# Kernel tuning notes

Hardware: AMD Instinct MI355X
Metric: run time of the kernel (lower is better)

The kernel has to match this reference:

```python
import jax, jax.numpy as jnp
import numpy as np

N, D, V, T = 1024, 64, 32000, 2048
U_DECAY = 0.97
LN_EPS = 1e-6


def _layernorm_row(z):
    # matches torch: (z - mean) / (std_unbiased + eps), std uses ddof=1
    m = z.mean(axis=-1, keepdims=True)
    s = jnp.std(z, axis=-1, ddof=1, keepdims=True)
    return (z - m) / (s + LN_EPS)


def setup_inputs() -> dict:
    key = jax.random.key(0)
    k1, k2, k3, k4, k5 = jax.random.split(key, 5)
    E = jax.random.normal(k1, (D, N), dtype=jnp.float32) / np.float32(np.sqrt(N))
    Dx = jax.random.normal(k2, (N, D), dtype=jnp.float32) / np.float32(np.sqrt(D))
    Dy = jax.random.normal(k3, (N, D), dtype=jnp.float32) / np.float32(np.sqrt(D))
    token_emb = jax.random.normal(k4, (V, D), dtype=jnp.float32) / np.float32(np.sqrt(D))
    tokens = jax.random.randint(k5, (T,), 0, V, dtype=jnp.int32)
    x0 = jnp.zeros((N,), dtype=jnp.float32)
    rho0 = jnp.zeros((D, N), dtype=jnp.float32)
    return {"E": E, "Dx": Dx, "Dy": Dy, "token_emb": token_emb,
            "x0": x0, "rho0": rho0, "tokens": tokens}


def reference(E, Dx, Dy, token_emb, x0, rho0, tokens):
    def step(carry, tok):
        x, rho = carry                        # x: [N], rho: [D, N]
        v_prev = token_emb[tok]               # [D]
        x_t = x + jax.nn.relu(Dx @ v_prev)    # [N], use_relu_lowrank=True
        a_star = rho @ x_t                    # [D]
        y_core = Dy @ _layernorm_row(a_star)  # ln_before_Dy=True -> [N]
        y_t = jax.nn.relu(y_core) * jax.nn.relu(x_t)  # [N]
        v_star = _layernorm_row(E @ y_t)      # [D]
        rho_new = U_DECAY * (rho + jnp.outer(v_prev, x_t))  # [D, N]
        return (x_t, rho_new), (y_t, v_star)

    (_, _), (ys, vs) = jax.lax.scan(step, (x0, rho0), tokens)
    return ys, vs  # [T, N], [T, D]
```

## Files before the change

kernel.cpp:

```cpp
#include <hip/hip_runtime.h>
#include <math.h>

#define NN 1024
#define DD 64
#define TT 2048
#define UDEC 0.97f
#define EPS 1e-6f
#define CC 64
#define NCH 32
#define NSL 8
#define SLW 128
#define C2 32
#define NC2 64

__global__ __launch_bounds__(256) void k_xscan(
    const float* __restrict__ Dx, const float* __restrict__ temb,
    const int* __restrict__ toks, float* __restrict__ Xp, float* __restrict__ S)
{
    const int cs = blockIdx.y;
    const int n  = blockIdx.x * 256 + threadIdx.x;
    __shared__ float Vs[C2][DD];
    for (int i = threadIdx.x; i < C2 * DD; i += 256) {
        int s = i >> 6, d = i & 63;
        Vs[s][d] = temb[toks[cs * C2 + s] * DD + d];
    }
    __syncthreads();
    float dxr[DD];
    const float4* dx4 = reinterpret_cast<const float4*>(Dx + n * DD);
#pragma unroll
    for (int j = 0; j < DD / 4; ++j) {
        float4 v = dx4[j];
        dxr[4*j] = v.x; dxr[4*j+1] = v.y; dxr[4*j+2] = v.z; dxr[4*j+3] = v.w;
    }
    float run = 0.f;
    for (int s = 0; s < C2; ++s) {
        const float4* vr = reinterpret_cast<const float4*>(&Vs[s][0]);
        float a0 = 0.f, a1 = 0.f, a2 = 0.f, a3 = 0.f;
#pragma unroll
        for (int j = 0; j < DD / 4; ++j) {
            float4 v = vr[j];
            a0 += v.x * dxr[4*j];     a1 += v.y * dxr[4*j+1];
            a2 += v.z * dxr[4*j+2];   a3 += v.w * dxr[4*j+3];
        }
        float r = (a0 + a1) + (a2 + a3);
        run += fmaxf(r, 0.f);
        Xp[(cs * C2 + s) * NN + n] = run;
    }
    S[cs * NN + n] = run;
}

__global__ __launch_bounds__(256) void k_base(
    const float* __restrict__ S, const float* __restrict__ x0, float* __restrict__ Bb)
{
    const int n = blockIdx.x * 256 + threadIdx.x;
    float acc = x0[n];
    for (int cs = 0; cs < NC2; ++cs) {
        Bb[cs * NN + n] = acc;
        acc += S[cs * NN + n];
    }
}


__global__ __launch_bounds__(256) void k_M(
    const float* __restrict__ Xp, const float* __restrict__ Bb,
    const float* __restrict__ temb, const int* __restrict__ toks, float* __restrict__ M)
{
    const int c = blockIdx.y, q = blockIdx.x;
    __shared__ float Xs[CC][SLW + 1];
    __shared__ float Vw[CC][DD];
    __shared__ float pw[CC + 1];
    const int tid = threadIdx.x;
    if (tid <= CC) pw[tid] = powf(UDEC, (float)tid);
    __syncthreads();
    for (int i = tid; i < CC * SLW; i += 256) {
        int s = i / SLW, n = i % SLW;
        int t = c * CC + s, gn = q * SLW + n;
        Xs[s][n] = Xp[t * NN + gn] + Bb[(t >> 5) * NN + gn];
    }
    for (int i = tid; i < CC * DD; i += 256) {
        int s = i >> 6, d = i & 63;
        Vw[s][d] = temb[toks[c * CC + s] * DD + d] * pw[CC - s];
    }
    __syncthreads();
    const int n_l = tid & 127;
    const int dh  = tid >> 7;
    float acc[32];
#pragma unroll
    for (int k = 0; k < 32; ++k) acc[k] = 0.f;
    for (int s = 0; s < CC; ++s) {
        float xv = Xs[s][n_l];
        const float4* vr = reinterpret_cast<const float4*>(&Vw[s][dh * 32]);
#pragma unroll
        for (int k8 = 0; k8 < 8; ++k8) {
            float4 v = vr[k8];
            acc[4*k8]   += v.x * xv;  acc[4*k8+1] += v.y * xv;
            acc[4*k8+2] += v.z * xv;  acc[4*k8+3] += v.w * xv;
        }
    }
    for (int k = 0; k < 32; ++k)
        M[(c * DD + dh * 32 + k) * NN + q * SLW + n_l] = acc[k];
}

__global__ __launch_bounds__(256) void k_rho(
    const float* __restrict__ M, const float* __restrict__ rho0, float* __restrict__ Rho)
{
    const int el = blockIdx.x * 256 + threadIdx.x;
    float acc = rho0[el];
    const float uc = powf(UDEC, (float)CC);
    for (int c = 0; c < NCH; ++c) {
        Rho[c * (DD * NN) + el] = acc;
        acc = fmaf(acc, uc, M[c * (DD * NN) + el]);
    }
}

__global__ __launch_bounds__(256) void k_gram(
    const float* __restrict__ Xp, const float* __restrict__ Bb,
    const float* __restrict__ Rho, float* __restrict__ Gp, float* __restrict__ Pp)
{
    const int c = blockIdx.y, q = blockIdx.x;
    __shared__ float Xs[CC][SLW + 1];
    __shared__ float Rs[DD][SLW + 1];
    const int tid = threadIdx.x;
    for (int i = tid; i < CC * SLW; i += 256) {
        int s = i / SLW, n = i % SLW;
        int t = c * CC + s, gn = q * SLW + n;
        Xs[s][n] = Xp[t * NN + gn] + Bb[(t >> 5) * NN + gn];
        Rs[s][n] = Rho[(c * DD + s) * NN + gn];
    }
    __syncthreads();
    const int ti = tid >> 4;
    const int sj = tid & 15;
    float acc[16];
#pragma unroll
    for (int k = 0; k < 16; ++k) acc[k] = 0.f;
    for (int n = 0; n < SLW; ++n) {
        float xt[4], xs[4];
#pragma unroll
        for (int a = 0; a < 4; ++a) xt[a] = Xs[ti * 4 + a][n];
#pragma unroll
        for (int b = 0; b < 4; ++b) xs[b] = Xs[sj * 4 + b][n];
#pragma unroll
        for (int a = 0; a < 4; ++a)
#pragma unroll
            for (int b = 0; b < 4; ++b) acc[a * 4 + b] += xt[a] * xs[b];
    }
    {
        float* base = Gp + ((size_t)(c * NSL + q) * CC) * CC;
#pragma unroll
        for (int a = 0; a < 4; ++a)
            *reinterpret_cast<float4*>(base + (ti * 4 + a) * CC + sj * 4) =
                make_float4(acc[a*4], acc[a*4+1], acc[a*4+2], acc[a*4+3]);
    }
#pragma unroll
    for (int k = 0; k < 16; ++k) acc[k] = 0.f;
    for (int n = 0; n < SLW; ++n) {
        float xt[4], rv[4];
#pragma unroll
        for (int a = 0; a < 4; ++a) xt[a] = Xs[ti * 4 + a][n];
#pragma unroll
        for (int b = 0; b < 4; ++b) rv[b] = Rs[sj * 4 + b][n];
#pragma unroll
        for (int a = 0; a < 4; ++a)
#pragma unroll
            for (int b = 0; b < 4; ++b) acc[a * 4 + b] += xt[a] * rv[b];
    }
    {
        float* base = Pp + ((size_t)(c * NSL + q) * CC) * DD;
#pragma unroll
        for (int a = 0; a < 4; ++a)
            *reinterpret_cast<float4*>(base + (ti * 4 + a) * DD + sj * 4) =
                make_float4(acc[a*4], acc[a*4+1], acc[a*4+2], acc[a*4+3]);
    }
}

__global__ __launch_bounds__(256) void k_astar(
    const float* __restrict__ Gp, const float* __restrict__ Pp,
    const float* __restrict__ temb, const int* __restrict__ toks,
    float* __restrict__ LNA)
{
    const int c = blockIdx.x;
    __shared__ float G[CC][CC + 1];
    __shared__ float P[CC][DD + 1];
    __shared__ float Ve[CC][DD];
    __shared__ float As[CC][DD + 1];
    __shared__ float pw[CC + 1];
    __shared__ float mrow[CC], srow[CC];
    const int tid = threadIdx.x;
    if (tid <= CC) pw[tid] = powf(UDEC, (float)tid);
    for (int i = tid; i < CC * CC; i += 256) {
        int t = i >> 6, s = i & 63;
        float ag = 0.f, ap = 0.f;
#pragma unroll
        for (int qq = 0; qq < NSL; ++qq) {
            ag += Gp[((size_t)(c * NSL + qq) * CC + t) * CC + s];
            ap += Pp[((size_t)(c * NSL + qq) * CC + t) * DD + s];
        }
        G[t][s] = ag; P[t][s] = ap;
    }
    for (int i = tid; i < CC * DD; i += 256) {
        int s = i >> 6, d = i & 63;
        Ve[s][d] = temb[toks[c * CC + s] * DD + d];
    }
    __syncthreads();
    const int t_l = tid >> 2;
    const int qq  = tid & 3;
    float acc[16];
#pragma unroll
    for (int j = 0; j < 16; ++j) acc[j] = pw[t_l] * P[t_l][qq * 16 + j];
    for (int s = 0; s < t_l; ++s) {
        float wv = pw[t_l - s] * G[t_l][s];
        const float4* ver = reinterpret_cast<const float4*>(&Ve[s][qq * 16]);
#pragma unroll
        for (int k = 0; k < 4; ++k) {
            float4 v = ver[k];
            acc[4*k]   += wv * v.x;  acc[4*k+1] += wv * v.y;
            acc[4*k+2] += wv * v.z;  acc[4*k+3] += wv * v.w;
        }
    }
#pragma unroll
    for (int j = 0; j < 16; ++j) As[t_l][qq * 16 + j] = acc[j];
    __syncthreads();
    if (tid < CC) {
        float m = 0.f;
#pragma unroll
        for (int d = 0; d < DD; ++d) m += As[tid][d];
        m *= (1.f / DD);
        float v = 0.f;
#pragma unroll
        for (int d = 0; d < DD; ++d) { float z = As[tid][d] - m; v += z * z; }
        mrow[tid] = m;
        srow[tid] = 1.f / (sqrtf(v / (DD - 1)) + EPS);
    }
    __syncthreads();
    for (int i = tid; i < CC * DD; i += 256) {
        int t = i >> 6, d = i & 63;
        LNA[(c * CC + t) * DD + d] = (As[t][d] - mrow[t]) * srow[t];
    }
}

__global__ __launch_bounds__(256) void k_y(
    const float* __restrict__ LNA, const float* __restrict__ Dy,
    const float* __restrict__ Xp, const float* __restrict__ Bb,
    float* __restrict__ ys)
{
    const int tt = blockIdx.y;
    const int n  = blockIdx.x * 256 + threadIdx.x;
    __shared__ float L[8][DD];
    for (int i = threadIdx.x; i < 8 * DD; i += 256) L[i >> 6][i & 63] = LNA[tt * 8 * DD + i];
    __syncthreads();
    float dyr[DD];
    const float4* dy4 = reinterpret_cast<const float4*>(Dy + n * DD);
#pragma unroll
    for (int j = 0; j < 16; ++j) {
        float4 v = dy4[j];
        dyr[4*j] = v.x; dyr[4*j+1] = v.y; dyr[4*j+2] = v.z; dyr[4*j+3] = v.w;
    }
#pragma unroll
    for (int t = 0; t < 8; ++t) {
        const float4* lr = reinterpret_cast<const float4*>(&L[t][0]);
        float a0 = 0.f, a1 = 0.f, a2 = 0.f, a3 = 0.f;
#pragma unroll
        for (int j = 0; j < 16; ++j) {
            float4 v = lr[j];
            a0 += v.x * dyr[4*j];   a1 += v.y * dyr[4*j+1];
            a2 += v.z * dyr[4*j+2]; a3 += v.w * dyr[4*j+3];
        }
        float yc = (a0 + a1) + (a2 + a3);
        int tg = tt * 8 + t;
        float xv = Xp[tg * NN + n] + Bb[(tg >> 5) * NN + n];
        ys[tg * NN + n] = fmaxf(yc, 0.f) * fmaxf(xv, 0.f);
    }
}

__global__ __launch_bounds__(256) void k_v(
    const float* __restrict__ ys, const float* __restrict__ E, float* __restrict__ vs)
{
    const int tt = blockIdx.x;
    __shared__ float Ys[8][NN];
    __shared__ float pre[8][DD + 1];
    __shared__ float mrow[8], srow[8];
    const int tid = threadIdx.x;
    for (int i = tid; i < 8 * NN; i += 256) Ys[i >> 10][i & 1023] = ys[tt * 8 * NN + i];
    __syncthreads();
    const int d  = tid & 63;
    const int tq = tid >> 6;
    const int t0 = tq * 2;
    const float4* e4 = reinterpret_cast<const float4*>(E + d * NN);
    float a00=0,a01=0,a02=0,a03=0, a10=0,a11=0,a12=0,a13=0;
    for (int j = 0; j < NN / 4; ++j) {
        float4 ev  = e4[j];
        float4 y0v = *reinterpret_cast<const float4*>(&Ys[t0][4 * j]);
        float4 y1v = *reinterpret_cast<const float4*>(&Ys[t0 + 1][4 * j]);
        a00 += ev.x * y0v.x; a01 += ev.y * y0v.y; a02 += ev.z * y0v.z; a03 += ev.w * y0v.w;
        a10 += ev.x * y1v.x; a11 += ev.y * y1v.y; a12 += ev.z * y1v.z; a13 += ev.w * y1v.w;
    }
    pre[t0][d]     = (a00 + a01) + (a02 + a03);
    pre[t0 + 1][d] = (a10 + a11) + (a12 + a13);
    __syncthreads();
    if (tid < 8) {
        float m = 0.f;
#pragma unroll
        for (int dd2 = 0; dd2 < DD; ++dd2) m += pre[tid][dd2];
        m *= (1.f / DD);
        float v = 0.f;
#pragma unroll
        for (int dd2 = 0; dd2 < DD; ++dd2) { float z = pre[tid][dd2] - m; v += z * z; }
        mrow[tid] = m;
        srow[tid] = 1.f / (sqrtf(v / (DD - 1)) + EPS);
    }
    __syncthreads();
    for (int i = tid; i < 8 * DD; i += 256) {
        int t = i >> 6, dd2 = i & 63;
        vs[(tt * 8 + t) * DD + dd2] = (pre[t][dd2] - mrow[t]) * srow[t];
    }
}

extern "C" void kernel_launch(void* const* d_in, const int* in_sizes, int n_in,
                              void* d_out, int out_size, void* d_ws, size_t ws_size,
                              hipStream_t stream) {
    (void)in_sizes; (void)n_in; (void)out_size; (void)ws_size;
    const float* E    = (const float*)d_in[0];
    const float* Dx   = (const float*)d_in[1];
    const float* Dy   = (const float*)d_in[2];
    const float* temb = (const float*)d_in[3];
    const float* x0   = (const float*)d_in[4];
    const float* rho0 = (const float*)d_in[5];
    const int*   toks = (const int*)d_in[6];

    float* ys = (float*)d_out;
    float* vs = ys + (size_t)TT * NN;

    float* w   = (float*)d_ws;
    float* Xp  = w;
    float* S   = Xp  + (size_t)TT * NN;
    float* Bb  = S   + (size_t)NC2 * NN;
    float* M   = Bb  + (size_t)NC2 * NN;
    float* Rho = M   + (size_t)NCH * DD * NN;
    float* LNA = Rho + (size_t)NCH * DD * NN;
    float* Gp = M;
    float* Pp = M + (size_t)NCH * NSL * CC * CC;

    k_xscan<<<dim3(4, NC2),  256, 0, stream>>>(Dx, temb, toks, Xp, S);
    k_base <<<dim3(4),       256, 0, stream>>>(S, x0, Bb);
    k_M    <<<dim3(NSL, NCH),256, 0, stream>>>(Xp, Bb, temb, toks, M);
    k_rho  <<<dim3(DD*NN/256),256,0, stream>>>(M, rho0, Rho);
    k_gram <<<dim3(NSL, NCH),256, 0, stream>>>(Xp, Bb, Rho, Gp, Pp);
    k_astar<<<dim3(NCH),     256, 0, stream>>>(Gp, Pp, temb, toks, LNA);
    k_y    <<<dim3(4, TT/8), 256, 0, stream>>>(LNA, Dy, Xp, Bb, ys);
    k_v    <<<dim3(TT/8),    256, 0, stream>>>(ys, E, vs);
}
```

Before: 194.7 us.

## Fuse all stages into one persistent kernel with grid-wide barriers

```diff
diff --git a/kernel.cpp b/kernel.cpp
--- a/kernel.cpp
+++ b/kernel.cpp
@@ -13,305 +13,297 @@
 #define C2 32
 #define NC2 64
 
-__global__ __launch_bounds__(256) void k_xscan(
-    const float* __restrict__ Dx, const float* __restrict__ temb,
-    const int* __restrict__ toks, float* __restrict__ Xp, float* __restrict__ S)
+#define NBLK 256
+#define NTHR 256
+
+struct SmP1 { float Vs[C2][DD]; };
+struct SmP3 { float Xs[CC][SLW + 1]; float Vw[CC][DD]; float pw[CC + 1]; };
+struct SmP5 { float Xs[CC][65]; float Rs[CC][65]; };
+struct SmP6 { float Ve[CC][DD]; float Gt[8][CC]; float Pt[8][DD]; float pw[CC + 1]; };
+struct SmP7 { float Ys[8][NN]; float L[8][DD]; float pre[8][DD + 1]; float mrow[8]; float srow[8]; };
+#define SMEM_BYTES 50176
+
+__device__ __forceinline__ void gridbar(unsigned* cnt, unsigned target) {
+    __syncthreads();
+    if (threadIdx.x == 0) {
+        __builtin_amdgcn_fence(__ATOMIC_RELEASE, "agent");
+        atomicAdd(cnt, 1u);
+        int spins = 0;
+        while (__hip_atomic_load(cnt, __ATOMIC_RELAXED, __HIP_MEMORY_SCOPE_AGENT) < target) {
+            __builtin_amdgcn_s_sleep(2);
+            if (++spins > (1 << 22)) break;
+        }
+        __builtin_amdgcn_fence(__ATOMIC_ACQUIRE, "agent");
+    }
+    __syncthreads();
+}
+
+__global__ __launch_bounds__(NTHR) void fused_bdh(
+    const float* __restrict__ E, const float* __restrict__ Dx,
+    const float* __restrict__ Dy, const float* __restrict__ temb,
+    const float* __restrict__ x0, const float* __restrict__ rho0,
+    const int* __restrict__ toks,
+    float* __restrict__ ys, float* __restrict__ vs,
+    float* __restrict__ Xp, float* __restrict__ S, float* __restrict__ Bb,
+    float* __restrict__ M, float* __restrict__ Rho, float* __restrict__ LNA,
+    float* __restrict__ Gp, float* __restrict__ Pp, unsigned* __restrict__ bar)
 {
-    const int cs = blockIdx.y;
-    const int n  = blockIdx.x * 256 + threadIdx.x;
-    __shared__ float Vs[C2][DD];
-    for (int i = threadIdx.x; i < C2 * DD; i += 256) {
-        int s = i >> 6, d = i & 63;
-        Vs[s][d] = temb[toks[cs * C2 + s] * DD + d];
-    }
-    __syncthreads();
-    float dxr[DD];
-    const float4* dx4 = reinterpret_cast<const float4*>(Dx + n * DD);
-#pragma unroll
-    for (int j = 0; j < DD / 4; ++j) {
-        float4 v = dx4[j];
-        dxr[4*j] = v.x; dxr[4*j+1] = v.y; dxr[4*j+2] = v.z; dxr[4*j+3] = v.w;
-    }
-    float run = 0.f;
-    for (int s = 0; s < C2; ++s) {
-        const float4* vr = reinterpret_cast<const float4*>(&Vs[s][0]);
-        float a0 = 0.f, a1 = 0.f, a2 = 0.f, a3 = 0.f;
-#pragma unroll
-        for (int j = 0; j < DD / 4; ++j) {
-            float4 v = vr[j];
-            a0 += v.x * dxr[4*j];     a1 += v.y * dxr[4*j+1];
-            a2 += v.z * dxr[4*j+2];   a3 += v.w * dxr[4*j+3];
-        }
-        float r = (a0 + a1) + (a2 + a3);
-        run += fmaxf(r, 0.f);
-        Xp[(cs * C2 + s) * NN + n] = run;
-    }
-    S[cs * NN + n] = run;
-}
-
-__global__ __launch_bounds__(256) void k_base(
-    const float* __restrict__ S, const float* __restrict__ x0, float* __restrict__ Bb)
-{
-    const int n = blockIdx.x * 256 + threadIdx.x;
-    float acc = x0[n];
-    for (int cs = 0; cs < NC2; ++cs) {
-        Bb[cs * NN + n] = acc;
-        acc += S[cs * NN + n];
-    }
-}
-
-
-__global__ __launch_bounds__(256) void k_M(
-    const float* __restrict__ Xp, const float* __restrict__ Bb,
-    const float* __restrict__ temb, const int* __restrict__ toks, float* __restrict__ M)
-{
-    const int c = blockIdx.y, q = blockIdx.x;
-    __shared__ float Xs[CC][SLW + 1];
-    __shared__ float Vw[CC][DD];
-    __shared__ float pw[CC + 1];
-    const int tid = threadIdx.x;
-    if (tid <= CC) pw[tid] = powf(UDEC, (float)tid);
-    __syncthreads();
-    for (int i = tid; i < CC * SLW; i += 256) {
-        int s = i / SLW, n = i % SLW;
-        int t = c * CC + s, gn = q * SLW + n;
-        Xs[s][n] = Xp[t * NN + gn] + Bb[(t >> 5) * NN + gn];
-    }
-    for (int i = tid; i < CC * DD; i += 256) {
-        int s = i >> 6, d = i & 63;
-        Vw[s][d] = temb[toks[c * CC + s] * DD + d] * pw[CC - s];
-    }
-    __syncthreads();
-    const int n_l = tid & 127;
-    const int dh  = tid >> 7;
-    float acc[32];
-#pragma unroll
-    for (int k = 0; k < 32; ++k) acc[k] = 0.f;
-    for (int s = 0; s < CC; ++s) {
-        float xv = Xs[s][n_l];
-        const float4* vr = reinterpret_cast<const float4*>(&Vw[s][dh * 32]);
-#pragma unroll
-        for (int k8 = 0; k8 < 8; ++k8) {
-            float4 v = vr[k8];
-            acc[4*k8]   += v.x * xv;  acc[4*k8+1] += v.y * xv;
-            acc[4*k8+2] += v.z * xv;  acc[4*k8+3] += v.w * xv;
-        }
-    }
-    for (int k = 0; k < 32; ++k)
-        M[(c * DD + dh * 32 + k) * NN + q * SLW + n_l] = acc[k];
-}
-
-__global__ __launch_bounds__(256) void k_rho(
-    const float* __restrict__ M, const float* __restrict__ rho0, float* __restrict__ Rho)
-{
-    const int el = blockIdx.x * 256 + threadIdx.x;
-    float acc = rho0[el];
-    const float uc = powf(UDEC, (float)CC);
-    for (int c = 0; c < NCH; ++c) {
-        Rho[c * (DD * NN) + el] = acc;
-        acc = fmaf(acc, uc, M[c * (DD * NN) + el]);
-    }
-}
-
-__global__ __launch_bounds__(256) void k_gram(
-    const float* __restrict__ Xp, const float* __restrict__ Bb,
-    const float* __restrict__ Rho, float* __restrict__ Gp, float* __restrict__ Pp)
-{
-    const int c = blockIdx.y, q = blockIdx.x;
-    __shared__ float Xs[CC][SLW + 1];
-    __shared__ float Rs[DD][SLW + 1];
-    const int tid = threadIdx.x;
-    for (int i = tid; i < CC * SLW; i += 256) {
-        int s = i / SLW, n = i % SLW;
-        int t = c * CC + s, gn = q * SLW + n;
-        Xs[s][n] = Xp[t * NN + gn] + Bb[(t >> 5) * NN + gn];
-        Rs[s][n] = Rho[(c * DD + s) * NN + gn];
-    }
-    __syncthreads();
-    const int ti = tid >> 4;
-    const int sj = tid & 15;
-    float acc[16];
-#pragma unroll
-    for (int k = 0; k < 16; ++k) acc[k] = 0.f;
-    for (int n = 0; n < SLW; ++n) {
-        float xt[4], xs[4];
-#pragma unroll
-        for (int a = 0; a < 4; ++a) xt[a] = Xs[ti * 4 + a][n];
-#pragma unroll
-        for (int b = 0; b < 4; ++b) xs[b] = Xs[sj * 4 + b][n];
-#pragma unroll
-        for (int a = 0; a < 4; ++a)
-#pragma unroll
-            for (int b = 0; b < 4; ++b) acc[a * 4 + b] += xt[a] * xs[b];
-    }
-    {
-        float* base = Gp + ((size_t)(c * NSL + q) * CC) * CC;
-#pragma unroll
-        for (int a = 0; a < 4; ++a)
-            *reinterpret_cast<float4*>(base + (ti * 4 + a) * CC + sj * 4) =
-                make_float4(acc[a*4], acc[a*4+1], acc[a*4+2], acc[a*4+3]);
-    }
-#pragma unroll
-    for (int k = 0; k < 16; ++k) acc[k] = 0.f;
-    for (int n = 0; n < SLW; ++n) {
-        float xt[4], rv[4];
-#pragma unroll
-        for (int a = 0; a < 4; ++a) xt[a] = Xs[ti * 4 + a][n];
-#pragma unroll
-        for (int b = 0; b < 4; ++b) rv[b] = Rs[sj * 4 + b][n];
-#pragma unroll
-        for (int a = 0; a < 4; ++a)
-#pragma unroll
-            for (int b = 0; b < 4; ++b) acc[a * 4 + b] += xt[a] * rv[b];
-    }
-    {
+    extern __shared__ __align__(16) char smem[];
+    const int b = blockIdx.x, tid = threadIdx.x;
+
+    {
+        SmP1* sm = (SmP1*)smem;
+        const int cs = b >> 2, qx = b & 3;
+        const int n = qx * 256 + tid;
+        for (int i = tid; i < C2 * DD; i += NTHR) {
+            int s = i >> 6, d = i & 63;
+            sm->Vs[s][d] = temb[toks[cs * C2 + s] * DD + d];
+        }
+        __syncthreads();
+        float dxr[DD];
+        const float4* dx4 = reinterpret_cast<const float4*>(Dx + n * DD);
+#pragma unroll
+        for (int j = 0; j < 16; ++j) {
+            float4 v = dx4[j];
+            dxr[4*j] = v.x; dxr[4*j+1] = v.y; dxr[4*j+2] = v.z; dxr[4*j+3] = v.w;
+        }
+        float run = 0.f;
+        for (int s = 0; s < C2; ++s) {
+            const float4* vr = reinterpret_cast<const float4*>(&sm->Vs[s][0]);
+            float a0 = 0.f, a1 = 0.f, a2 = 0.f, a3 = 0.f;
+#pragma unroll
+            for (int j = 0; j < 16; ++j) {
+                float4 v = vr[j];
+                a0 += v.x * dxr[4*j];     a1 += v.y * dxr[4*j+1];
+                a2 += v.z * dxr[4*j+2];   a3 += v.w * dxr[4*j+3];
+            }
+            run += fmaxf((a0 + a1) + (a2 + a3), 0.f);
+            Xp[(cs * C2 + s) * NN + n] = run;
+        }
+        S[cs * NN + n] = run;
+    }
+    gridbar(bar, 1 * NBLK);
+
+    if (b < 4) {
+        const int n = b * 256 + tid;
+        float acc = x0[n];
+        for (int cs = 0; cs < NC2; ++cs) {
+            Bb[cs * NN + n] = acc;
+            acc += S[cs * NN + n];
+        }
+    }
+    gridbar(bar, 2 * NBLK);
+
+    {
+        SmP3* sm = (SmP3*)smem;
+        const int c = b >> 3, q = b & 7;
+        if (tid <= CC) sm->pw[tid] = powf(UDEC, (float)tid);
+        __syncthreads();
+        for (int i = tid; i < CC * SLW; i += NTHR) {
+            int s = i >> 7, n = i & 127;
+            int t = c * CC + s, gn = q * SLW + n;
+            sm->Xs[s][n] = Xp[t * NN + gn] + Bb[(t >> 5) * NN + gn];
+        }
+        for (int i = tid; i < CC * DD; i += NTHR) {
+            int s = i >> 6, d = i & 63;
+            sm->Vw[s][d] = temb[toks[c * CC + s] * DD + d] * sm->pw[CC - s];
+        }
+        __syncthreads();
+        {
+            const int n_l = tid & 127, dh = tid >> 7;
+            float acc[32];
+#pragma unroll
+            for (int k = 0; k < 32; ++k) acc[k] = 0.f;
+            for (int s = 0; s < CC; ++s) {
+                float xv = sm->Xs[s][n_l];
+                const float4* vr = reinterpret_cast<const float4*>(&sm->Vw[s][dh * 32]);
+#pragma unroll
+                for (int k8 = 0; k8 < 8; ++k8) {
+                    float4 v = vr[k8];
+                    acc[4*k8]   += v.x * xv;  acc[4*k8+1] += v.y * xv;
+                    acc[4*k8+2] += v.z * xv;  acc[4*k8+3] += v.w * xv;
+                }
+            }
+            for (int k = 0; k < 32; ++k)
+                M[(c * DD + dh * 32 + k) * NN + q * SLW + n_l] = acc[k];
+        }
+        {
+            const int ti = tid >> 4, sj = tid & 15;
+            float acc[16];
+#pragma unroll
+            for (int k = 0; k < 16; ++k) acc[k] = 0.f;
+            for (int n = 0; n < SLW; ++n) {
+                float xt[4], xs[4];
+#pragma unroll
+                for (int a = 0; a < 4; ++a) xt[a] = sm->Xs[ti * 4 + a][n];
+#pragma unroll
+                for (int e2 = 0; e2 < 4; ++e2) xs[e2] = sm->Xs[sj * 4 + e2][n];
+#pragma unroll
+                for (int a = 0; a < 4; ++a)
+#pragma unroll
+                    for (int e2 = 0; e2 < 4; ++e2) acc[a * 4 + e2] += xt[a] * xs[e2];
+            }
+            float* base = Gp + ((size_t)(c * NSL + q) * CC) * CC;
+#pragma unroll
+            for (int a = 0; a < 4; ++a)
+                *reinterpret_cast<float4*>(base + (ti * 4 + a) * CC + sj * 4) =
+                    make_float4(acc[a*4], acc[a*4+1], acc[a*4+2], acc[a*4+3]);
+        }
+    }
+    gridbar(bar, 3 * NBLK);
+
+    {
+        const int el = b * NTHR + tid;
+        float acc = rho0[el];
+        const float uc = powf(UDEC, (float)CC);
+        for (int c = 0; c < NCH; ++c) {
+            Rho[c * (DD * NN) + el] = acc;
+            acc = fmaf(acc, uc, M[c * (DD * NN) + el]);
+        }
+    }
+    gridbar(bar, 4 * NBLK);
+
+    {
+        SmP5* sm = (SmP5*)smem;
+        const int c = b >> 3, q = b & 7;
+        const int ti = tid >> 4, sj = tid & 15;
+        float acc[16];
+#pragma unroll
+        for (int k = 0; k < 16; ++k) acc[k] = 0.f;
+        for (int h = 0; h < 2; ++h) {
+            __syncthreads();
+            for (int i = tid; i < CC * 64; i += NTHR) {
+                int s = i >> 6, n = i & 63;
+                int t = c * CC + s, gn = q * SLW + h * 64 + n;
+                sm->Xs[s][n] = Xp[t * NN + gn] + Bb[(t >> 5) * NN + gn];
+                sm->Rs[s][n] = Rho[(c * DD + s) * NN + gn];
+            }
+            __syncthreads();
+            for (int n = 0; n < 64; ++n) {
+                float xt[4], rv[4];
+#pragma unroll
+                for (int a = 0; a < 4; ++a) xt[a] = sm->Xs[ti * 4 + a][n];
+#pragma unroll
+                for (int e2 = 0; e2 < 4; ++e2) rv[e2] = sm->Rs[sj * 4 + e2][n];
+#pragma unroll
+                for (int a = 0; a < 4; ++a)
+#pragma unroll
+                    for (int e2 = 0; e2 < 4; ++e2) acc[a * 4 + e2] += xt[a] * rv[e2];
+            }
+        }
         float* base = Pp + ((size_t)(c * NSL + q) * CC) * DD;
 #pragma unroll
         for (int a = 0; a < 4; ++a)
             *reinterpret_cast<float4*>(base + (ti * 4 + a) * DD + sj * 4) =
                 make_float4(acc[a*4], acc[a*4+1], acc[a*4+2], acc[a*4+3]);
     }
-}
-
-__global__ __launch_bounds__(256) void k_astar(
-    const float* __restrict__ Gp, const float* __restrict__ Pp,
-    const float* __restrict__ temb, const int* __restrict__ toks,
-    float* __restrict__ LNA)
-{
-    const int c = blockIdx.x;
-    __shared__ float G[CC][CC + 1];
-    __shared__ float P[CC][DD + 1];
-    __shared__ float Ve[CC][DD];
-    __shared__ float As[CC][DD + 1];
-    __shared__ float pw[CC + 1];
-    __shared__ float mrow[CC], srow[CC];
-    const int tid = threadIdx.x;
-    if (tid <= CC) pw[tid] = powf(UDEC, (float)tid);
-    for (int i = tid; i < CC * CC; i += 256) {
-        int t = i >> 6, s = i & 63;
-        float ag = 0.f, ap = 0.f;
-#pragma unroll
-        for (int qq = 0; qq < NSL; ++qq) {
-            ag += Gp[((size_t)(c * NSL + qq) * CC + t) * CC + s];
-            ap += Pp[((size_t)(c * NSL + qq) * CC + t) * DD + s];
-        }
-        G[t][s] = ag; P[t][s] = ap;
-    }
-    for (int i = tid; i < CC * DD; i += 256) {
-        int s = i >> 6, d = i & 63;
-        Ve[s][d] = temb[toks[c * CC + s] * DD + d];
-    }
-    __syncthreads();
-    const int t_l = tid >> 2;
-    const int qq  = tid & 3;
-    float acc[16];
-#pragma unroll
-    for (int j = 0; j < 16; ++j) acc[j] = pw[t_l] * P[t_l][qq * 16 + j];
-    for (int s = 0; s < t_l; ++s) {
-        float wv = pw[t_l - s] * G[t_l][s];
-        const float4* ver = reinterpret_cast<const float4*>(&Ve[s][qq * 16]);
-#pragma unroll
-        for (int k = 0; k < 4; ++k) {
-            float4 v = ver[k];
-            acc[4*k]   += wv * v.x;  acc[4*k+1] += wv * v.y;
-            acc[4*k+2] += wv * v.z;  acc[4*k+3] += wv * v.w;
-        }
-    }
-#pragma unroll
-    for (int j = 0; j < 16; ++j) As[t_l][qq * 16 + j] = acc[j];
-    __syncthreads();
-    if (tid < CC) {
-        float m = 0.f;
-#pragma unroll
-        for (int d = 0; d < DD; ++d) m += As[tid][d];
-        m *= (1.f / DD);
-        float v = 0.f;
-#pragma unroll
-        for (int d = 0; d < DD; ++d) { float z = As[tid][d] - m; v += z * z; }
-        mrow[tid] = m;
-        srow[tid] = 1.f / (sqrtf(v / (DD - 1)) + EPS);
-    }
-    __syncthreads();
-    for (int i = tid; i < CC * DD; i += 256) {
-        int t = i >> 6, d = i & 63;
-        LNA[(c * CC + t) * DD + d] = (As[t][d] - mrow[t]) * srow[t];
-    }
-}
-
-__global__ __launch_bounds__(256) void k_y(
-    const float* __restrict__ LNA, const float* __restrict__ Dy,
-    const float* __restrict__ Xp, const float* __restrict__ Bb,
-    float* __restrict__ ys)
-{
-    const int tt = blockIdx.y;
-    const int n  = blockIdx.x * 256 + threadIdx.x;
-    __shared__ float L[8][DD];
-    for (int i = threadIdx.x; i < 8 * DD; i += 256) L[i >> 6][i & 63] = LNA[tt * 8 * DD + i];
-    __syncthreads();
-    float dyr[DD];
-    const float4* dy4 = reinterpret_cast<const float4*>(Dy + n * DD);
-#pragma unroll
-    for (int j = 0; j < 16; ++j) {
-        float4 v = dy4[j];
-        dyr[4*j] = v.x; dyr[4*j+1] = v.y; dyr[4*j+2] = v.z; dyr[4*j+3] = v.w;
-    }
-#pragma unroll
-    for (int t = 0; t < 8; ++t) {
-        const float4* lr = reinterpret_cast<const float4*>(&L[t][0]);
-        float a0 = 0.f, a1 = 0.f, a2 = 0.f, a3 = 0.f;
-#pragma unroll
-        for (int j = 0; j < 16; ++j) {
-            float4 v = lr[j];
-            a0 += v.x * dyr[4*j];   a1 += v.y * dyr[4*j+1];
-            a2 += v.z * dyr[4*j+2]; a3 += v.w * dyr[4*j+3];
-        }
-        float yc = (a0 + a1) + (a2 + a3);
-        int tg = tt * 8 + t;
-        float xv = Xp[tg * NN + n] + Bb[(tg >> 5) * NN + n];
-        ys[tg * NN + n] = fmaxf(yc, 0.f) * fmaxf(xv, 0.f);
-    }
-}
-
-__global__ __launch_bounds__(256) void k_v(
-    const float* __restrict__ ys, const float* __restrict__ E, float* __restrict__ vs)
-{
-    const int tt = blockIdx.x;
-    __shared__ float Ys[8][NN];
-    __shared__ float pre[8][DD + 1];
-    __shared__ float mrow[8], srow[8];
-    const int tid = threadIdx.x;
-    for (int i = tid; i < 8 * NN; i += 256) Ys[i >> 10][i & 1023] = ys[tt * 8 * NN + i];
-    __syncthreads();
-    const int d  = tid & 63;
-    const int tq = tid >> 6;
-    const int t0 = tq * 2;
-    const float4* e4 = reinterpret_cast<const float4*>(E + d * NN);
-    float a00=0,a01=0,a02=0,a03=0, a10=0,a11=0,a12=0,a13=0;
-    for (int j = 0; j < NN / 4; ++j) {
-        float4 ev  = e4[j];
-        float4 y0v = *reinterpret_cast<const float4*>(&Ys[t0][4 * j]);
-        float4 y1v = *reinterpret_cast<const float4*>(&Ys[t0 + 1][4 * j]);
-        a00 += ev.x * y0v.x; a01 += ev.y * y0v.y; a02 += ev.z * y0v.z; a03 += ev.w * y0v.w;
-        a10 += ev.x * y1v.x; a11 += ev.y * y1v.y; a12 += ev.z * y1v.z; a13 += ev.w * y1v.w;
-    }
-    pre[t0][d]     = (a00 + a01) + (a02 + a03);
-    pre[t0 + 1][d] = (a10 + a11) + (a12 + a13);
-    __syncthreads();
-    if (tid < 8) {
-        float m = 0.f;
-#pragma unroll
-        for (int dd2 = 0; dd2 < DD; ++dd2) m += pre[tid][dd2];
-        m *= (1.f / DD);
-        float v = 0.f;
-#pragma unroll
-        for (int dd2 = 0; dd2 < DD; ++dd2) { float z = pre[tid][dd2] - m; v += z * z; }
-        mrow[tid] = m;
-        srow[tid] = 1.f / (sqrtf(v / (DD - 1)) + EPS);
-    }
-    __syncthreads();
-    for (int i = tid; i < 8 * DD; i += 256) {
-        int t = i >> 6, dd2 = i & 63;
-        vs[(tt * 8 + t) * DD + dd2] = (pre[t][dd2] - mrow[t]) * srow[t];
+    gridbar(bar, 5 * NBLK);
+
+    {
+        SmP6* sm = (SmP6*)smem;
+        const int c = b >> 3, sub = b & 7;
+        if (tid <= CC) sm->pw[tid] = powf(UDEC, (float)tid);
+        for (int i = tid; i < CC * DD; i += NTHR) {
+            int s = i >> 6, d = i & 63;
+            sm->Ve[s][d] = temb[toks[c * CC + s] * DD + d];
+        }
+        for (int i = tid; i < 8 * CC; i += NTHR) {
+            int k = i >> 6, s = i & 63;
+            int t = sub + 8 * k;
+            float ag = 0.f, ap = 0.f;
+#pragma unroll
+            for (int q = 0; q < NSL; ++q) {
+                ag += Gp[((size_t)(c * NSL + q) * CC + t) * CC + s];
+                ap += Pp[((size_t)(c * NSL + q) * CC + t) * DD + s];
+            }
+            sm->Gt[k][s] = ag; sm->Pt[k][s] = ap;
+        }
+        __syncthreads();
+        const int tk = tid >> 5, d0 = tid & 31;
+        const int t = sub + 8 * tk;
+        float a0 = sm->pw[t] * sm->Pt[tk][d0];
+        float a1 = sm->pw[t] * sm->Pt[tk][d0 + 32];
+        for (int s = 0; s < t; ++s) {
+            float w = sm->pw[t - s] * sm->Gt[tk][s];
+            a0 += w * sm->Ve[s][d0];
+            a1 += w * sm->Ve[s][d0 + 32];
+        }
+        float sum = a0 + a1;
+#pragma unroll
+        for (int m = 1; m < 32; m <<= 1) sum += __shfl_xor(sum, m, 32);
+        float mean = sum * (1.f / DD);
+        float z0 = a0 - mean, z1 = a1 - mean;
+        float vsum = z0 * z0 + z1 * z1;
+#pragma unroll
+        for (int m = 1; m < 32; m <<= 1) vsum += __shfl_xor(vsum, m, 32);
+        float inv = 1.f / (sqrtf(vsum * (1.f / (DD - 1))) + EPS);
+        LNA[(c * CC + t) * DD + d0]      = z0 * inv;
+        LNA[(c * CC + t) * DD + d0 + 32] = z1 * inv;
+    }
+    gridbar(bar, 6 * NBLK);
+
+    {
+        SmP7* sm = (SmP7*)smem;
+        const int tt = b;
+        for (int i = tid; i < 8 * DD; i += NTHR) sm->L[i >> 6][i & 63] = LNA[tt * 8 * DD + i];
+        __syncthreads();
+        for (int nq = 0; nq < 4; ++nq) {
+            const int n = nq * 256 + tid;
+            float dyr[DD];
+            const float4* dy4 = reinterpret_cast<const float4*>(Dy + n * DD);
+#pragma unroll
+            for (int j = 0; j < 16; ++j) {
+                float4 v = dy4[j];
+                dyr[4*j] = v.x; dyr[4*j+1] = v.y; dyr[4*j+2] = v.z; dyr[4*j+3] = v.w;
+            }
+#pragma unroll
+            for (int t = 0; t < 8; ++t) {
+                const float4* lr = reinterpret_cast<const float4*>(&sm->L[t][0]);
+                float a0 = 0.f, a1 = 0.f, a2 = 0.f, a3 = 0.f;
+#pragma unroll
+                for (int j = 0; j < 16; ++j) {
+                    float4 v = lr[j];
+                    a0 += v.x * dyr[4*j];   a1 += v.y * dyr[4*j+1];
+                    a2 += v.z * dyr[4*j+2]; a3 += v.w * dyr[4*j+3];
+                }
+                float yc = (a0 + a1) + (a2 + a3);
+                int tg = tt * 8 + t;
+                float xv = Xp[tg * NN + n] + Bb[(tg >> 5) * NN + n];
+                float yv = fmaxf(yc, 0.f) * fmaxf(xv, 0.f);
+                ys[tg * NN + n] = yv;
+                sm->Ys[t][n] = yv;
+            }
+        }
+        __syncthreads();
+        const int d = tid & 63, tq = tid >> 6, t0 = tq * 2;
+        const float4* e4 = reinterpret_cast<const float4*>(E + d * NN);
+        float a00=0,a01=0,a02=0,a03=0, a10=0,a11=0,a12=0,a13=0;
+        for (int j = 0; j < NN / 4; ++j) {
+            float4 ev  = e4[j];
+            float4 y0v = *reinterpret_cast<const float4*>(&sm->Ys[t0][4 * j]);
+            float4 y1v = *reinterpret_cast<const float4*>(&sm->Ys[t0 + 1][4 * j]);
+            a00 += ev.x * y0v.x; a01 += ev.y * y0v.y; a02 += ev.z * y0v.z; a03 += ev.w * y0v.w;
+            a10 += ev.x * y1v.x; a11 += ev.y * y1v.y; a12 += ev.z * y1v.z; a13 += ev.w * y1v.w;
+        }
+        sm->pre[t0][d]     = (a00 + a01) + (a02 + a03);
+        sm->pre[t0 + 1][d] = (a10 + a11) + (a12 + a13);
+        __syncthreads();
+        if (tid < 8) {
+            float m = 0.f;
+#pragma unroll
+            for (int dd2 = 0; dd2 < DD; ++dd2) m += sm->pre[tid][dd2];
+            m *= (1.f / DD);
+            float v = 0.f;
+#pragma unroll
+            for (int dd2 = 0; dd2 < DD; ++dd2) { float z = sm->pre[tid][dd2] - m; v += z * z; }
+            sm->mrow[tid] = m;
+            sm->srow[tid] = 1.f / (sqrtf(v * (1.f / (DD - 1))) + EPS);
+        }
+        __syncthreads();
+        for (int i = tid; i < 8 * DD; i += NTHR) {
+            int t = i >> 6, dd2 = i & 63;
+            vs[(tt * 8 + t) * DD + dd2] = (sm->pre[t][dd2] - sm->mrow[t]) * sm->srow[t];
+        }
     }
 }
 
@@ -337,15 +329,12 @@
     float* M   = Bb  + (size_t)NC2 * NN;
     float* Rho = M   + (size_t)NCH * DD * NN;
     float* LNA = Rho + (size_t)NCH * DD * NN;
-    float* Gp = M;
-    float* Pp = M + (size_t)NCH * NSL * CC * CC;
-
-    k_xscan<<<dim3(4, NC2),  256, 0, stream>>>(Dx, temb, toks, Xp, S);
-    k_base <<<dim3(4),       256, 0, stream>>>(S, x0, Bb);
-    k_M    <<<dim3(NSL, NCH),256, 0, stream>>>(Xp, Bb, temb, toks, M);
-    k_rho  <<<dim3(DD*NN/256),256,0, stream>>>(M, rho0, Rho);
-    k_gram <<<dim3(NSL, NCH),256, 0, stream>>>(Xp, Bb, Rho, Gp, Pp);
-    k_astar<<<dim3(NCH),     256, 0, stream>>>(Gp, Pp, temb, toks, LNA);
-    k_y    <<<dim3(4, TT/8), 256, 0, stream>>>(LNA, Dy, Xp, Bb, ys);
-    k_v    <<<dim3(TT/8),    256, 0, stream>>>(ys, E, vs);
+    float* Gp  = LNA + (size_t)TT * DD;
+    float* Pp  = Gp  + (size_t)NCH * NSL * CC * CC;
+    unsigned* bar = (unsigned*)(Pp + (size_t)NCH * NSL * CC * DD);
+
+    hipMemsetAsync(bar, 0, 64, stream);
+    hipLaunchKernelGGL(fused_bdh, dim3(NBLK), dim3(NTHR), SMEM_BYTES, stream,
+                       E, Dx, Dy, temb, x0, rho0, toks, ys, vs,
+                       Xp, S, Bb, M, Rho, LNA, Gp, Pp, bar);
 }
```

After: 279.2 us. 1.43x slower.
